# Optimization experiments

Measured on AMD Instinct MI355X. Metric: run time of the kernel, lower is better.

Reference implementation:

```python
import jax, jax.numpy as jnp
import numpy as np

nA = 4096; nB = 4096; C = 128; H = 4; D = 32; E = 65536
EPS = 1e-5


def _ln(x, g, b):
    m = jnp.mean(x, axis=-1, keepdims=True)
    v = jnp.var(x, axis=-1, keepdims=True)
    return (x - m) / jnp.sqrt(v + EPS) * g + b


def setup_inputs() -> dict:
    key = jax.random.key(0)
    ks = jax.random.split(key, 16)
    w = 0.02
    inp = {}
    inp["x_a"] = jax.random.normal(ks[0], (nA, C), dtype=jnp.float32)
    inp["x_b"] = jax.random.normal(ks[1], (nB, C), dtype=jnp.float32)
    inp["edge_ab"] = jax.random.randint(ks[2], (2, E), 0, nA)  # row0: src in A, row1: dst in B
    inp["edge_ba"] = jax.random.randint(ks[3], (2, E), 0, nB)  # row0: src in B, row1: dst in A
    inp["Wq"] = jax.random.normal(ks[4], (C, C), dtype=jnp.float32) * w
    inp["bq"] = jnp.zeros((C,), jnp.float32)
    inp["Wk"] = jax.random.normal(ks[5], (C, C), dtype=jnp.float32) * w
    inp["bk"] = jnp.zeros((C,), jnp.float32)
    inp["Wv"] = jax.random.normal(ks[6], (C, C), dtype=jnp.float32) * w
    inp["bv"] = jnp.zeros((C,), jnp.float32)
    inp["Wo"] = jax.random.normal(ks[7], (C, C), dtype=jnp.float32) * w
    inp["bo"] = jnp.zeros((C,), jnp.float32)
    inp["g_attn"] = jnp.ones((C,), jnp.float32)   # pre_ln_attn
    inp["b_attn"] = jnp.zeros((C,), jnp.float32)
    inp["g_ffn"] = jnp.ones((C,), jnp.float32)    # pre_ln_ffn
    inp["b_ffn"] = jnp.zeros((C,), jnp.float32)
    inp["g_f"] = jnp.ones((C,), jnp.float32)      # LayerNorm inside ffn Sequential
    inp["b_f"] = jnp.zeros((C,), jnp.float32)
    inp["W1"] = jax.random.normal(ks[8], (C, C), dtype=jnp.float32) * w
    inp["b1"] = jnp.zeros((C,), jnp.float32)
    inp["W2"] = jax.random.normal(ks[9], (C, C), dtype=jnp.float32) * w
    inp["b2"] = jnp.zeros((C,), jnp.float32)
    inp["rel_ab"] = jax.random.normal(ks[10], (1,), dtype=jnp.float32)
    inp["rel_ba"] = jax.random.normal(ks[11], (1,), dtype=jnp.float32)
    return inp


def reference(x_a, x_b, edge_ab, edge_ba, Wq, bq, Wk, bk, Wv, bv, Wo, bo,
              g_attn, b_attn, g_ffn, b_ffn, g_f, b_f, W1, b1, W2, b2,
              rel_ab, rel_ba):
    inv_sqrt_d = 1.0 / jnp.sqrt(jnp.float32(D))

    def all_pairs_attn(xq, xkv, rel):
        nQ, nK = xq.shape[0], xkv.shape[0]
        Q = (xq @ Wq + bq).reshape(nQ, H, D)
        K = (xkv @ Wk + bk).reshape(nK, H, D)
        V = (xkv @ Wv + bv).reshape(nK, H, D)
        # [nQ, nK, H] logits with additive relation bias
        logits = jnp.einsum('ihd,jhd->ijh', Q, K) * inv_sqrt_d + rel
        a = jax.nn.softmax(logits, axis=1)  # softmax over all source nodes per dst
        return jnp.einsum('ijh,jhd->ihd', a, V).reshape(nQ, C)

    xn_a = _ln(x_a, g_attn, b_attn)
    xn_b = _ln(x_b, g_attn, b_attn)
    # edge type B->A contributes to dst type A; A->B to dst type B
    attn_a = all_pairs_attn(xn_a, xn_b, rel_ba[0]) @ Wo + bo
    attn_b = all_pairs_attn(xn_b, xn_a, rel_ab[0]) @ Wo + bo

    # total degree = out-degree + in-degree across edge types (eval: dropout = identity)
    ones = jnp.ones((E,), jnp.float32)
    deg_a = jax.ops.segment_sum(ones, edge_ab[0], num_segments=nA) + \
            jax.ops.segment_sum(ones, edge_ba[1], num_segments=nA)
    deg_b = jax.ops.segment_sum(ones, edge_ba[0], num_segments=nB) + \
            jax.ops.segment_sum(ones, edge_ab[1], num_segments=nB)
    attn_a = attn_a + deg_a[:, None]
    attn_b = attn_b + deg_b[:, None]

    res_a = x_a + attn_a
    res_b = x_b + attn_b

    def ffn(xr):
        h = _ln(xr, g_ffn, b_ffn)        # pre_ln_ffn
        h = _ln(h, g_f, b_f)             # LayerNorm inside ffn Sequential
        h = jax.nn.gelu(h @ W1 + b1, approximate=False)
        return h @ W2 + b2

    out_a = res_a + ffn(res_a)
    out_b = res_b + ffn(res_b)
    return jnp.stack([out_a, out_b])  # [2, n, C]
```

## Files before the change

### kernel.cpp

```cpp
#include <hip/hip_runtime.h>

typedef unsigned short u16;
typedef unsigned int   u32;
typedef __attribute__((ext_vector_type(8))) short bf16x8;
typedef __attribute__((ext_vector_type(4))) float f32x4;

#define NEL (8192*128)

#define ASYNC16(ldsptr, gptr) __builtin_amdgcn_global_load_lds( \
    (const __attribute__((address_space(1))) u32*)(gptr), \
    (__attribute__((address_space(3))) u32*)(ldsptr), 16, 0, 0)

__device__ __forceinline__ u16 f2bf(float f){
  u32 u = __builtin_bit_cast(u32, f);
  u = (u + 0x7FFFu + ((u >> 16) & 1u)) >> 16;
  return (u16)u;
}
__device__ __forceinline__ u32 pk2(float a, float b){
  u32 r;
  asm("v_cvt_pk_bf16_f32 %0, %1, %2" : "=v"(r) : "v"(a), "v"(b));
  return r;
}

__global__ __launch_bounds__(256) void prep_kernel(
    const int* __restrict__ eab, const int* __restrict__ eba, float* __restrict__ partial,
    const float* __restrict__ Wq, const float* __restrict__ Wk, const float* __restrict__ Wv,
    const float* __restrict__ Wo, const float* __restrict__ W1, const float* __restrict__ W2,
    u16* __restrict__ WT)
{
  __shared__ u32 hist[8192];
  __shared__ float tile[32][33];
  const int b = blockIdx.x, t = threadIdx.x;
  if (b < 64){
    #pragma unroll
    for (int i=0;i<32;i++) hist[t + i*256] = 0u;
    __syncthreads();
    const int e0 = b*1024;
    #pragma unroll
    for (int i=0;i<4;i++){
      int e = e0 + t + i*256;
      atomicAdd(&hist[eab[e]],              1u);
      atomicAdd(&hist[4096 + eab[65536+e]], 1u);
      atomicAdd(&hist[4096 + eba[e]],       1u);
      atomicAdd(&hist[eba[65536+e]],        1u);
    }
    __syncthreads();
    #pragma unroll
    for (int i=0;i<32;i++){
      int bin = t + i*256;
      partial[b*8192 + bin] = (float)hist[bin];
    }
  } else {
    int id = b - 64;
    int w = id >> 4, tt = id & 15, tr = tt >> 2, tc = tt & 3;
    const float* W = (w==0)?Wq:(w==1)?Wk:(w==2)?Wv:(w==3)?Wo:(w==4)?W1:W2;
    int r = t >> 3, c4 = (t&7)*4;
    float4 v = *(const float4*)(W + (tr*32 + r)*128 + tc*32 + c4);
    tile[r][c4]=v.x; tile[r][c4+1]=v.y; tile[r][c4+2]=v.z; tile[r][c4+3]=v.w;
    __syncthreads();
    int n = t >> 3, k4 = (t&7)*4;
    u32 lo = pk2(tile[k4+0][n], tile[k4+1][n]);
    u32 hi = pk2(tile[k4+2][n], tile[k4+3][n]);
    *(uint2*)(WT + w*16384 + (tc*32+n)*128 + tr*32 + k4) = make_uint2(lo, hi);
  }
}

__global__ __launch_bounds__(512) void ln_qkv_kernel(
    const float* __restrict__ xa, const float* __restrict__ xb,
    const float* __restrict__ g, const float* __restrict__ bvec,
    const u16* __restrict__ WT,
    const float* __restrict__ bq, const float* __restrict__ bk, const float* __restrict__ bv,
    const float* __restrict__ partial, float* __restrict__ deg,
    u16* __restrict__ Qb, u16* __restrict__ Kb, u16* __restrict__ VT)
{
  __shared__ float xs[16][132];
  __shared__ __align__(16) u16 abf[16][128];
  __shared__ __align__(16) u16 vtb[128][24];
  const int t = threadIdx.x, lane = t&63, wave = t>>6;
  const int lq = lane&15, lg = lane>>4;
  const int row0 = blockIdx.x*16;
  const float* x = (row0 < 4096) ? (xa + row0*128) : (xb + (row0-4096)*128);
  if (t < 16){
    int bin = blockIdx.x*16 + t;
    float s = 0.f;
    #pragma unroll
    for (int j=0;j<64;j++) s += partial[j*8192 + bin];
    deg[bin] = s;
  }
  {
    int r = t>>5, c4 = (t&31)*4;
    float4 v = *(const float4*)(x + r*128 + c4);
    xs[r][c4]=v.x; xs[r][c4+1]=v.y; xs[r][c4+2]=v.z; xs[r][c4+3]=v.w;
  }
  __syncthreads();
  if (t < 256){
    int r = t>>4, c0 = t&15;
    float s=0.f, s2=0.f;
    #pragma unroll
    for (int j=0;j<8;j++){ float v = xs[r][c0+j*16]; s+=v; s2+=v*v; }
    #pragma unroll
    for (int m=1;m<16;m<<=1){ s += __shfl_xor(s,m); s2 += __shfl_xor(s2,m); }
    float mean = s*0.0078125f;
    float var  = s2*0.0078125f - mean*mean;
    float rstd = rsqrtf(var + 1e-5f);
    #pragma unroll
    for (int j=0;j<8;j++){
      int c = c0 + j*16;
      float h = (xs[r][c]-mean)*rstd*g[c] + bvec[c];
      int sj = (c>>3) ^ (r&7);
      abf[r][sj*8 + (c&7)] = f2bf(h);
    }
  }
  __syncthreads();
  bf16x8 af[4];
  #pragma unroll
  for (int s=0;s<4;s++){
    int sj = (s*4+lg) ^ (lq&7);
    af[s] = *(const bf16x8*)&abf[lq][sj*8];
  }
  const int cb = wave*16;
  const float QSC = 0.17677669529663687f * 1.4426950408889634f;
  #pragma unroll
  for (int m=0;m<3;m++){
    const u16* Wg = WT + m*16384;
    bf16x8 bfr[4];
    #pragma unroll
    for (int s=0;s<4;s++)
      bfr[s] = *(const bf16x8*)(Wg + (cb+lq)*128 + s*32 + lg*8);
    f32x4 acc = {0,0,0,0};
    #pragma unroll
    for (int s=0;s<4;s++)
      acc = __builtin_amdgcn_mfma_f32_16x16x32_bf16(af[s], bfr[s], acc, 0,0,0);
    int col = cb + lq;
    if (m==0){
      float bb = bq[col];
      #pragma unroll
      for (int r=0;r<4;r++)
        Qb[(row0+4*lg+r)*128 + col] = f2bf((acc[r]+bb)*QSC);
    } else if (m==1){
      float bb = bk[col];
      #pragma unroll
      for (int r=0;r<4;r++)
        Kb[(row0+4*lg+r)*128 + col] = f2bf(acc[r]+bb);
    } else {
      float bb = bv[col];
      #pragma unroll
      for (int r=0;r<4;r++)
        vtb[col][4*lg+r] = f2bf(acc[r]+bb);
    }
  }
  __syncthreads();
  if (t < 256){
    int c = t>>1, half = t&1;
    bf16x8 v = *(const bf16x8*)&vtb[c][half*8];
    *(bf16x8*)(VT + c*8192 + row0 + half*8) = v;
  }
}

__global__ __launch_bounds__(256) void attn_kernel(
    const u16* __restrict__ Qb, const u16* __restrict__ Kb,
    const u16* __restrict__ VT, float* __restrict__ numb, float* __restrict__ denb)
{
  __shared__ __align__(16) u16 Klds[3][2048];
  __shared__ __align__(16) u16 Vlds[3][2048];
  __shared__ __align__(16) u16 Plds[4][1024];
  const int t = threadIdx.x, wave = t>>6, lane = t&63;
  const int lq = lane&15, lg = lane>>4;
  const int h = blockIdx.y;
  const int dir = blockIdx.z >> 2, sp = blockIdx.z & 3;
  const int q = blockIdx.x*64 + wave*16 + lq + (dir ? 4096 : 0);
  const int kvb = (dir ? 0 : 4096) + sp*1024;

  bf16x8 qf = *(const bf16x8*)(Qb + q*128 + h*32 + lg*8);
  f32x4 acc0 = {0,0,0,0}, acc1 = {0,0,0,0}, accL = {0,0,0,0};
  bf16x8 ones;
  #pragma unroll
  for (int i=0;i<8;i++) ones[i] = (short)0x3F80;

  const u16* gk = Kb + (kvb + (t>>2))*128 + h*32 + ((t&3) ^ ((t>>3)&3))*8;
  const u16* gv = VT + (h*32 + (t>>3))*8192 + kvb + ((t&7) ^ ((t>>3)&7))*8;

  ASYNC16(&Klds[0][t*8], gk);
  ASYNC16(&Vlds[0][t*8], gv);
  ASYNC16(&Klds[1][t*8], gk + 8192);
  ASYNC16(&Vlds[1][t*8], gv + 64);

  #pragma unroll
  for (int kt=0; kt<16; ++kt){
    const int cur = kt % 3;
    if (kt == 15) asm volatile("s_waitcnt vmcnt(0)" ::: "memory");
    else          asm volatile("s_waitcnt vmcnt(2)" ::: "memory");
    __builtin_amdgcn_s_barrier();
    __builtin_amdgcn_sched_barrier(0);
    if (kt < 14){
      const int nb = (kt+2) % 3;
      ASYNC16(&Klds[nb][t*8], gk + (kt+2)*8192);
      ASYNC16(&Vlds[nb][t*8], gv + (kt+2)*64);
    }
    const u16* KL = Klds[cur];
    const u16* VL = Vlds[cur];
    u16* PL = Plds[wave] + lq*64;
    const int ksj = lg ^ ((lq>>1)&3);
    #pragma unroll
    for (int f=0; f<4; ++f){
      bf16x8 kf = *(const bf16x8*)(KL + (f*16+lq)*32 + ksj*8);
      f32x4 st = __builtin_amdgcn_mfma_f32_16x16x32_bf16(kf, qf, (f32x4){0.f,0.f,0.f,0.f}, 0,0,0);
      float p0 = __builtin_amdgcn_exp2f(st[0]);
      float p1 = __builtin_amdgcn_exp2f(st[1]);
      float p2 = __builtin_amdgcn_exp2f(st[2]);
      float p3 = __builtin_amdgcn_exp2f(st[3]);
      int j = f*2 + (lg>>1);
      *(uint2*)(PL + ((j ^ (lq&7))<<3) + (lg&1)*4) = make_uint2(pk2(p0,p1), pk2(p2,p3));
    }
    __builtin_amdgcn_s_setprio(1);
    #pragma unroll
    for (int kc=0; kc<2; ++kc){
      int sj = (kc*4+lg) ^ (lq&7);
      bf16x8 pf  = *(const bf16x8*)(PL + (sj<<3));
      bf16x8 vf0 = *(const bf16x8*)(VL + lq*64      + (sj<<3));
      bf16x8 vf1 = *(const bf16x8*)(VL + (16+lq)*64 + (sj<<3));
      acc0 = __builtin_amdgcn_mfma_f32_16x16x32_bf16(vf0,  pf, acc0, 0,0,0);
      acc1 = __builtin_amdgcn_mfma_f32_16x16x32_bf16(vf1,  pf, acc1, 0,0,0);
      accL = __builtin_amdgcn_mfma_f32_16x16x32_bf16(ones, pf, accL, 0,0,0);
    }
    __builtin_amdgcn_s_setprio(0);
  }
  float* outp = numb + sp*NEL + q*128 + h*32 + 4*lg;
  *(float4*)(outp)      = make_float4(acc0[0], acc0[1], acc0[2], acc0[3]);
  *(float4*)(outp + 16) = make_float4(acc1[0], acc1[1], acc1[2], acc1[3]);
  if (lg == 0) denb[sp*32768 + q*4 + h] = accL[0];
}

__global__ __launch_bounds__(512) void tail_kernel(
    const float* __restrict__ numb, const float* __restrict__ denb,
    const u16* __restrict__ WT,
    const float* __restrict__ bo, const float* __restrict__ deg,
    const float* __restrict__ xa, const float* __restrict__ xb,
    const float* __restrict__ gf1, const float* __restrict__ bf1,
    const float* __restrict__ gf2, const float* __restrict__ bf2,
    const float* __restrict__ b1, const float* __restrict__ b2,
    float* __restrict__ out)
{
  __shared__ __align__(16) u16 abf[16][128];
  __shared__ float rs[16][132];
  const int t = threadIdx.x, lane = t&63, wave = t>>6;
  const int lq = lane&15, lg = lane>>4;
  const int row0 = blockIdx.x*16;
  const int cb = wave*16;

  {
    int r = t>>5, c0 = (t&31)*4, hh = c0>>5;
    const float* np = numb + (row0+r)*128 + c0;
    float4 s0 = *(const float4*)(np);
    float4 s1 = *(const float4*)(np + NEL);
    float4 s2 = *(const float4*)(np + 2*NEL);
    float4 s3 = *(const float4*)(np + 3*NEL);
    int di = (row0+r)*4 + hh;
    float den = denb[di] + denb[32768+di] + denb[65536+di] + denb[98304+di];
    float inv = 1.0f/den;
    float a0 = (s0.x+s1.x+s2.x+s3.x)*inv;
    float a1 = (s0.y+s1.y+s2.y+s3.y)*inv;
    float a2 = (s0.z+s1.z+s2.z+s3.z)*inv;
    float a3 = (s0.w+s1.w+s2.w+s3.w)*inv;
    int sj = (c0>>3) ^ (r&7);
    *(uint2*)&abf[r][sj*8 + (c0&7)] = make_uint2(pk2(a0,a1), pk2(a2,a3));
  }
  __syncthreads();

  bf16x8 af[4];
  #pragma unroll
  for (int s=0;s<4;s++){ int sj = (s*4+lg) ^ (lq&7); af[s] = *(const bf16x8*)&abf[lq][sj*8]; }

  f32x4 acc = {0,0,0,0};
  {
    const u16* Wg = WT + 3*16384;
    bf16x8 bfr[4];
    #pragma unroll
    for (int s=0;s<4;s++) bfr[s] = *(const bf16x8*)(Wg + (cb+lq)*128 + s*32 + lg*8);
    #pragma unroll
    for (int s=0;s<4;s++) acc = __builtin_amdgcn_mfma_f32_16x16x32_bf16(af[s], bfr[s], acc, 0,0,0);
  }
  const float* xres = (row0<4096)? (xa + row0*128) : (xb + (row0-4096)*128);
  const int col = cb + lq;
  float rv[4];
  {
    float bb = bo[col];
    #pragma unroll
    for (int r=0;r<4;r++){
      int lr = 4*lg + r;
      rv[r] = acc[r] + bb + deg[row0+lr] + xres[lr*128 + col];
      rs[lr][col] = rv[r];
    }
  }
  __syncthreads();
  if (t < 256){
    int r = t>>4, c0 = t&15;
    float s=0.f, s2=0.f;
    #pragma unroll
    for (int j=0;j<8;j++){ float v = rs[r][c0+j*16]; s+=v; s2+=v*v; }
    #pragma unroll
    for (int m=1;m<16;m<<=1){ s += __shfl_xor(s,m); s2 += __shfl_xor(s2,m); }
    float mean = s*0.0078125f;
    float var  = s2*0.0078125f - mean*mean;
    float rstd = rsqrtf(var + 1e-5f);
    float h8[8];
    #pragma unroll
    for (int j=0;j<8;j++){ int c=c0+j*16; h8[j] = (rs[r][c]-mean)*rstd*gf1[c] + bf1[c]; }
    s=0.f; s2=0.f;
    #pragma unroll
    for (int j=0;j<8;j++){ s+=h8[j]; s2+=h8[j]*h8[j]; }
    #pragma unroll
    for (int m=1;m<16;m<<=1){ s += __shfl_xor(s,m); s2 += __shfl_xor(s2,m); }
    float mean2 = s*0.0078125f;
    float var2  = s2*0.0078125f - mean2*mean2;
    float rstd2 = rsqrtf(var2 + 1e-5f);
    #pragma unroll
    for (int j=0;j<8;j++){
      int c = c0 + j*16;
      float h = (h8[j]-mean2)*rstd2*gf2[c] + bf2[c];
      int sj = (c>>3) ^ (r&7);
      abf[r][sj*8 + (c&7)] = f2bf(h);
    }
  }
  __syncthreads();
  #pragma unroll
  for (int s=0;s<4;s++){ int sj = (s*4+lg) ^ (lq&7); af[s] = *(const bf16x8*)&abf[lq][sj*8]; }
  acc = (f32x4){0,0,0,0};
  {
    const u16* Wg = WT + 4*16384;
    bf16x8 bfr[4];
    #pragma unroll
    for (int s=0;s<4;s++) bfr[s] = *(const bf16x8*)(Wg + (cb+lq)*128 + s*32 + lg*8);
    #pragma unroll
    for (int s=0;s<4;s++) acc = __builtin_amdgcn_mfma_f32_16x16x32_bf16(af[s], bfr[s], acc, 0,0,0);
  }
  float gvv[4];
  {
    float bb = b1[col];
    #pragma unroll
    for (int r=0;r<4;r++){
      float v = acc[r] + bb;
      gvv[r] = 0.5f*v*(1.f + erff(v*0.70710678118654752f));
    }
  }
  __syncthreads();
  #pragma unroll
  for (int r=0;r<4;r++){
    int lr = 4*lg + r;
    int sj = (col>>3) ^ (lr&7);
    abf[lr][sj*8 + (col&7)] = f2bf(gvv[r]);
  }
  __syncthreads();
  #pragma unroll
  for (int s=0;s<4;s++){ int sj = (s*4+lg) ^ (lq&7); af[s] = *(const bf16x8*)&abf[lq][sj*8]; }
  acc = (f32x4){0,0,0,0};
  {
    const u16* Wg = WT + 5*16384;
    bf16x8 bfr[4];
    #pragma unroll
    for (int s=0;s<4;s++) bfr[s] = *(const bf16x8*)(Wg + (cb+lq)*128 + s*32 + lg*8);
    #pragma unroll
    for (int s=0;s<4;s++) acc = __builtin_amdgcn_mfma_f32_16x16x32_bf16(af[s], bfr[s], acc, 0,0,0);
  }
  {
    float bb = b2[col];
    #pragma unroll
    for (int r=0;r<4;r++){
      int lr = 4*lg + r;
      out[(row0+lr)*128 + col] = acc[r] + bb + rv[r];
    }
  }
}

extern "C" void kernel_launch(void* const* d_in, const int* in_sizes, int n_in,
                              void* d_out, int out_size, void* d_ws, size_t ws_size,
                              hipStream_t stream) {
  const float* xa  = (const float*)d_in[0];
  const float* xb  = (const float*)d_in[1];
  const int*   eab = (const int*)d_in[2];
  const int*   eba = (const int*)d_in[3];
  const float* Wq  = (const float*)d_in[4];   const float* bq = (const float*)d_in[5];
  const float* Wk  = (const float*)d_in[6];   const float* bk = (const float*)d_in[7];
  const float* Wv  = (const float*)d_in[8];   const float* bv = (const float*)d_in[9];
  const float* Wo  = (const float*)d_in[10];  const float* bo = (const float*)d_in[11];
  const float* ga  = (const float*)d_in[12];  const float* ba = (const float*)d_in[13];
  const float* gfn = (const float*)d_in[14];  const float* bfn= (const float*)d_in[15];
  const float* gf  = (const float*)d_in[16];  const float* bf = (const float*)d_in[17];
  const float* W1  = (const float*)d_in[18];  const float* b1 = (const float*)d_in[19];
  const float* W2  = (const float*)d_in[20];  const float* b2 = (const float*)d_in[21];
  float* out = (float*)d_out;

  char* w = (char*)d_ws;
  float* deg  = (float*)w;
  u16*   WT   = (u16*)(w + 32768);
  u16*   Qb   = (u16*)(w + 32768 + 196608);
  u16*   Kb   = Qb + NEL;
  u16*   VT   = Kb + NEL;
  float* numb = (float*)(VT + NEL);
  float* denb = numb + 4*NEL;
  float* partial = numb;

  prep_kernel<<<160, 256, 0, stream>>>(eab, eba, partial, Wq, Wk, Wv, Wo, W1, W2, WT);
  ln_qkv_kernel<<<512, 512, 0, stream>>>(xa, xb, ga, ba, WT, bq, bk, bv,
                                         partial, deg, Qb, Kb, VT);
  attn_kernel<<<dim3(64,4,8), 256, 0, stream>>>(Qb, Kb, VT, numb, denb);
  tail_kernel<<<512, 512, 0, stream>>>(numb, denb, WT, bo, deg, xa, xb,
                                       gfn, bfn, gf, bf, b1, b2, out);
}
```

Measured before the change: 180.2 us.

## Rewrite attention with 32x32x16 MFMA, register-resident P and 128-key double-buffered tiles

The attention kernel now uses 32x32x16 bf16 MFMAs, so each wave handles 32 queries. The score-to-P conversion stays in registers through v_permlane32_swap instead of a round trip through an LDS P buffer. K/V tiles grow to 128 keys, with double buffering replacing the triple-buffered 64-key pipeline, and the grid is halved. The aim is to remove LDS traffic and barriers per key and to reuse each K/V fragment across more queries. In exchange it uses more accumulator registers, waits on a full vmcnt(0) each tile, and adds occupancy hint 4.

```diff
diff --git a/kernel.cpp b/kernel.cpp
--- a/kernel.cpp
+++ b/kernel.cpp
@@ -4,6 +4,8 @@
 typedef unsigned int   u32;
 typedef __attribute__((ext_vector_type(8))) short bf16x8;
 typedef __attribute__((ext_vector_type(4))) float f32x4;
+typedef __attribute__((ext_vector_type(16))) float f32x16;
+typedef __attribute__((ext_vector_type(4))) u32 u32x4;
 
 #define NEL (8192*128)
 
@@ -157,78 +159,96 @@
   }
 }
 
-__global__ __launch_bounds__(256) void attn_kernel(
+__global__ __launch_bounds__(256, 4) void attn_kernel(
     const u16* __restrict__ Qb, const u16* __restrict__ Kb,
     const u16* __restrict__ VT, float* __restrict__ numb, float* __restrict__ denb)
 {
-  __shared__ __align__(16) u16 Klds[3][2048];
-  __shared__ __align__(16) u16 Vlds[3][2048];
-  __shared__ __align__(16) u16 Plds[4][1024];
+  __shared__ __align__(16) u16 Klds[2][4096];
+  __shared__ __align__(16) u16 Vlds[2][4096];
   const int t = threadIdx.x, wave = t>>6, lane = t&63;
-  const int lq = lane&15, lg = lane>>4;
+  const int lo5 = lane & 31, hi = lane >> 5;
   const int h = blockIdx.y;
   const int dir = blockIdx.z >> 2, sp = blockIdx.z & 3;
-  const int q = blockIdx.x*64 + wave*16 + lq + (dir ? 4096 : 0);
+  const int q = blockIdx.x*128 + wave*32 + lo5 + (dir ? 4096 : 0);
   const int kvb = (dir ? 0 : 4096) + sp*1024;
 
-  bf16x8 qf = *(const bf16x8*)(Qb + q*128 + h*32 + lg*8);
-  f32x4 acc0 = {0,0,0,0}, acc1 = {0,0,0,0}, accL = {0,0,0,0};
+  bf16x8 qB0 = *(const bf16x8*)(Qb + q*128 + h*32 + hi*8);
+  bf16x8 qB1 = *(const bf16x8*)(Qb + q*128 + h*32 + 16 + hi*8);
+
+  f32x16 acc  = {0,0,0,0,0,0,0,0,0,0,0,0,0,0,0,0};
+  f32x16 accL = {0,0,0,0,0,0,0,0,0,0,0,0,0,0,0,0};
   bf16x8 ones;
   #pragma unroll
   for (int i=0;i<8;i++) ones[i] = (short)0x3F80;
 
-  const u16* gk = Kb + (kvb + (t>>2))*128 + h*32 + ((t&3) ^ ((t>>3)&3))*8;
-  const u16* gv = VT + (h*32 + (t>>3))*8192 + kvb + ((t&7) ^ ((t>>3)&7))*8;
-
-  ASYNC16(&Klds[0][t*8], gk);
-  ASYNC16(&Vlds[0][t*8], gv);
-  ASYNC16(&Klds[1][t*8], gk + 8192);
-  ASYNC16(&Vlds[1][t*8], gv + 64);
-
-  #pragma unroll
-  for (int kt=0; kt<16; ++kt){
-    const int cur = kt % 3;
-    if (kt == 15) asm volatile("s_waitcnt vmcnt(0)" ::: "memory");
-    else          asm volatile("s_waitcnt vmcnt(2)" ::: "memory");
-    __builtin_amdgcn_s_barrier();
-    __builtin_amdgcn_sched_barrier(0);
-    if (kt < 14){
-      const int nb = (kt+2) % 3;
-      ASYNC16(&Klds[nb][t*8], gk + (kt+2)*8192);
-      ASYNC16(&Vlds[nb][t*8], gv + (kt+2)*64);
+  const u16* gk = Kb + (kvb + (t>>2))*128 + h*32 + (((t&3) ^ ((t>>3)&3))<<3);
+  const u16* gv = VT + (h*32 + (t>>4))*8192 + kvb + (((t&15) ^ ((t>>4)&7))<<3);
+
+  ASYNC16(&Klds[0][t*8],      gk);
+  ASYNC16(&Klds[0][t*8+2048], gk + 8192);
+  ASYNC16(&Vlds[0][t*8],      gv);
+  ASYNC16(&Vlds[0][t*8+2048], gv + 131072);
+  asm volatile("s_waitcnt vmcnt(0)" ::: "memory");
+  __builtin_amdgcn_s_barrier();
+
+  for (int kt=0; kt<8; ++kt){
+    const int cur = kt & 1;
+    if (kt < 7){
+      const u16* nk = gk + (kt+1)*16384;
+      const u16* nv = gv + (kt+1)*128;
+      ASYNC16(&Klds[cur^1][t*8],      nk);
+      ASYNC16(&Klds[cur^1][t*8+2048], nk + 8192);
+      ASYNC16(&Vlds[cur^1][t*8],      nv);
+      ASYNC16(&Vlds[cur^1][t*8+2048], nv + 131072);
     }
     const u16* KL = Klds[cur];
     const u16* VL = Vlds[cur];
-    u16* PL = Plds[wave] + lq*64;
-    const int ksj = lg ^ ((lq>>1)&3);
-    #pragma unroll
-    for (int f=0; f<4; ++f){
-      bf16x8 kf = *(const bf16x8*)(KL + (f*16+lq)*32 + ksj*8);
-      f32x4 st = __builtin_amdgcn_mfma_f32_16x16x32_bf16(kf, qf, (f32x4){0.f,0.f,0.f,0.f}, 0,0,0);
-      float p0 = __builtin_amdgcn_exp2f(st[0]);
-      float p1 = __builtin_amdgcn_exp2f(st[1]);
-      float p2 = __builtin_amdgcn_exp2f(st[2]);
-      float p3 = __builtin_amdgcn_exp2f(st[3]);
-      int j = f*2 + (lg>>1);
-      *(uint2*)(PL + ((j ^ (lq&7))<<3) + (lg&1)*4) = make_uint2(pk2(p0,p1), pk2(p2,p3));
-    }
-    __builtin_amdgcn_s_setprio(1);
-    #pragma unroll
-    for (int kc=0; kc<2; ++kc){
-      int sj = (kc*4+lg) ^ (lq&7);
-      bf16x8 pf  = *(const bf16x8*)(PL + (sj<<3));
-      bf16x8 vf0 = *(const bf16x8*)(VL + lq*64      + (sj<<3));
-      bf16x8 vf1 = *(const bf16x8*)(VL + (16+lq)*64 + (sj<<3));
-      acc0 = __builtin_amdgcn_mfma_f32_16x16x32_bf16(vf0,  pf, acc0, 0,0,0);
-      acc1 = __builtin_amdgcn_mfma_f32_16x16x32_bf16(vf1,  pf, acc1, 0,0,0);
-      accL = __builtin_amdgcn_mfma_f32_16x16x32_bf16(ones, pf, accL, 0,0,0);
-    }
-    __builtin_amdgcn_s_setprio(0);
-  }
-  float* outp = numb + sp*NEL + q*128 + h*32 + 4*lg;
-  *(float4*)(outp)      = make_float4(acc0[0], acc0[1], acc0[2], acc0[3]);
-  *(float4*)(outp + 16) = make_float4(acc1[0], acc1[1], acc1[2], acc1[3]);
-  if (lg == 0) denb[sp*32768 + q*4 + h] = accL[0];
+    const int dsw = lo5 & 7;
+    #pragma unroll
+    for (int k4=0; k4<4; ++k4){
+      const int key = k4*32 + lo5;
+      const int ksw = (key>>1)&3;
+      bf16x8 kA0 = *(const bf16x8*)(KL + key*32 + ((hi     ^ ksw)<<3));
+      bf16x8 kA1 = *(const bf16x8*)(KL + key*32 + (((2+hi) ^ ksw)<<3));
+      f32x16 st = __builtin_amdgcn_mfma_f32_32x32x16_bf16(kA0, qB0,
+                  (f32x16){0,0,0,0,0,0,0,0,0,0,0,0,0,0,0,0}, 0,0,0);
+      st = __builtin_amdgcn_mfma_f32_32x32x16_bf16(kA1, qB1, st, 0,0,0);
+      float p[16];
+      #pragma unroll
+      for (int r=0;r<16;r++) p[r] = __builtin_amdgcn_exp2f(st[r]);
+      u32 a0 = pk2(p[0],p[1]),  b0 = pk2(p[4],p[5]);
+      u32 c0 = pk2(p[2],p[3]),  d0 = pk2(p[6],p[7]);
+      asm("v_permlane32_swap_b32 %0, %1" : "+v"(b0), "+v"(a0));
+      asm("v_permlane32_swap_b32 %0, %1" : "+v"(d0), "+v"(c0));
+      u32x4 u0 = {a0, c0, b0, d0};
+      bf16x8 pf0 = __builtin_bit_cast(bf16x8, u0);
+      u32 a1 = pk2(p[8],p[9]),   b1 = pk2(p[12],p[13]);
+      u32 c1 = pk2(p[10],p[11]), d1 = pk2(p[14],p[15]);
+      asm("v_permlane32_swap_b32 %0, %1" : "+v"(b1), "+v"(a1));
+      asm("v_permlane32_swap_b32 %0, %1" : "+v"(d1), "+v"(c1));
+      u32x4 u1 = {a1, c1, b1, d1};
+      bf16x8 pf1 = __builtin_bit_cast(bf16x8, u1);
+      bf16x8 vA0 = *(const bf16x8*)(VL + lo5*128 + (((k4*4   + hi) ^ dsw)<<3));
+      bf16x8 vA1 = *(const bf16x8*)(VL + lo5*128 + (((k4*4+2 + hi) ^ dsw)<<3));
+      __builtin_amdgcn_s_setprio(1);
+      acc  = __builtin_amdgcn_mfma_f32_32x32x16_bf16(vA0,  pf0, acc,  0,0,0);
+      accL = __builtin_amdgcn_mfma_f32_32x32x16_bf16(ones, pf0, accL, 0,0,0);
+      acc  = __builtin_amdgcn_mfma_f32_32x32x16_bf16(vA1,  pf1, acc,  0,0,0);
+      accL = __builtin_amdgcn_mfma_f32_32x32x16_bf16(ones, pf1, accL, 0,0,0);
+      __builtin_amdgcn_s_setprio(0);
+    }
+    if (kt < 7){
+      asm volatile("s_waitcnt vmcnt(0)" ::: "memory");
+      __builtin_amdgcn_s_barrier();
+    }
+  }
+  float* o = numb + sp*NEL + q*128 + h*32;
+  #pragma unroll
+  for (int rg=0; rg<4; ++rg){
+    int d0 = 8*rg + 4*hi;
+    *(float4*)(o + d0) = make_float4(acc[rg*4+0], acc[rg*4+1], acc[rg*4+2], acc[rg*4+3]);
+  }
+  if (hi == 0) denb[sp*32768 + q*4 + h] = accL[0];
 }
 
 __global__ __launch_bounds__(512) void tail_kernel(
@@ -403,7 +423,7 @@
   prep_kernel<<<160, 256, 0, stream>>>(eab, eba, partial, Wq, Wk, Wv, Wo, W1, W2, WT);
   ln_qkv_kernel<<<512, 512, 0, stream>>>(xa, xb, ga, ba, WT, bq, bk, bv,
                                          partial, deg, Qb, Kb, VT);
-  attn_kernel<<<dim3(64,4,8), 256, 0, stream>>>(Qb, Kb, VT, numb, denb);
+  attn_kernel<<<dim3(32,4,8), 256, 0, stream>>>(Qb, Kb, VT, numb, denb);
   tail_kernel<<<512, 512, 0, stream>>>(numb, denb, WT, bo, deg, xa, xb,
                                        gfn, bfn, gf, bf, b1, b2, out);
 }
```

New measurement: 174.7 us. 3.1% less time.
